# Optimization experiments

Hardware: AMD Instinct MI355X
Metric: run time of the kernel (lower is better)

Reference implementation:

```python
import jax, jax.numpy as jnp
import numpy as np

B, T, D, H, O = 1024, 256, 63, 128, 14


def _lstm_dir(x, W_ih, W_hh, b_ih, b_hh):
    """Single-direction LSTM over x [B,T,D] -> hidden outputs [B,T,H].
    PyTorch gate order: i, f, g, o."""
    # Precompute input projection for all timesteps (one big GEMM).
    xp = x @ W_ih.T + (b_ih + b_hh)  # [B,T,4H]

    def step(carry, xt):
        h, c = carry
        gates = xt + h @ W_hh.T  # [B,4H]
        i, f, g, o = jnp.split(gates, 4, axis=-1)
        i = jax.nn.sigmoid(i)
        f = jax.nn.sigmoid(f)
        g = jnp.tanh(g)
        o = jax.nn.sigmoid(o)
        c = f * c + i * g
        h = o * jnp.tanh(c)
        return (h, c), h

    h0 = jnp.zeros((x.shape[0], W_hh.shape[1]), x.dtype)
    (_, _), hs = jax.lax.scan(step, (h0, h0), jnp.swapaxes(xp, 0, 1))
    return jnp.swapaxes(hs, 0, 1)  # [B,T,H]


def setup_inputs() -> dict:
    key = jax.random.key(0)
    ks = jax.random.split(key, 11)
    s = 1.0 / np.sqrt(H)  # PyTorch LSTM init scale
    return {
        "x": jax.random.normal(ks[0], (B, T, D), jnp.float32),
        "W_ih_f": jax.random.uniform(ks[1], (4 * H, D), jnp.float32, -s, s),
        "W_hh_f": jax.random.uniform(ks[2], (4 * H, H), jnp.float32, -s, s),
        "b_ih_f": jax.random.uniform(ks[3], (4 * H,), jnp.float32, -s, s),
        "b_hh_f": jax.random.uniform(ks[4], (4 * H,), jnp.float32, -s, s),
        "W_ih_b": jax.random.uniform(ks[5], (4 * H, D), jnp.float32, -s, s),
        "W_hh_b": jax.random.uniform(ks[6], (4 * H, H), jnp.float32, -s, s),
        "b_ih_b": jax.random.uniform(ks[7], (4 * H,), jnp.float32, -s, s),
        "b_hh_b": jax.random.uniform(ks[8], (4 * H,), jnp.float32, -s, s),
        "W_fc": jax.random.uniform(ks[9], (O, 2 * H), jnp.float32, -s, s),
        "b_fc": jax.random.uniform(ks[10], (O,), jnp.float32, -s, s),
    }


def reference(x, W_ih_f, W_hh_f, b_ih_f, b_hh_f,
              W_ih_b, W_hh_b, b_ih_b, b_hh_b, W_fc, b_fc):
    h_f = _lstm_dir(x, W_ih_f, W_hh_f, b_ih_f, b_hh_f)            # fwd dir
    h_b = _lstm_dir(x[:, ::-1], W_ih_b, W_hh_b, b_ih_b, b_hh_b)[:, ::-1]  # bwd dir
    # out[:, -1, :] of the BiLSTM; dropout is identity at inference.
    last = jnp.concatenate([h_f[:, -1], h_b[:, -1]], axis=-1)  # [B, 2H]
    return last @ W_fc.T + b_fc  # [B, O]
```

## Files before the change

kernel.cpp:

```cpp
#include <hip/hip_runtime.h>

typedef __attribute__((ext_vector_type(8))) short bf16x8;
typedef __attribute__((ext_vector_type(4))) float f32x4;

#define BB 1024
#define TT 256
#define DD 63
#define HH 128
#define CHUNK 4
#define HSTR 160
#define XSTR 96

#define LDS_BARRIER() asm volatile("s_waitcnt lgkmcnt(0)\n\ts_barrier" ::: "memory")

__device__ __forceinline__ short f2bf(float f) {
  unsigned u = __builtin_bit_cast(unsigned, f);
  u = (u + 0x7FFFu + ((u >> 16) & 1u)) >> 16;
  return (short)u;
}
__device__ __forceinline__ float sigm(float x) {
  return __builtin_amdgcn_rcpf(1.f + __expf(-x));
}
__device__ __forceinline__ float tanh_fast(float x) {
  float e = __expf(2.f * x);
  return 1.f - 2.f * __builtin_amdgcn_rcpf(e + 1.f);
}

__global__ __launch_bounds__(512, 2)
void bilstm_fused_kernel(const float* __restrict__ X,
                         const float* __restrict__ Wih,
                         const float* __restrict__ Whh,
                         const float* __restrict__ bih,
                         const float* __restrict__ bhh,
                         const float* __restrict__ Wih_b,
                         const float* __restrict__ bih_b,
                         const float* __restrict__ bhh_b,
                         const float* __restrict__ Wfc,
                         const float* __restrict__ bfc,
                         float* __restrict__ out) {
  __shared__ __align__(16) short hbuf[2 * 4 * HSTR];
  __shared__ __align__(16) short xbuf[2 * 4 * XSTR];
  __shared__ __align__(16) float fst[4 * 256];
  __shared__ __align__(16) float xl[4 * 64];
  __shared__ __align__(16) float glb[4 * 512];

  const int tid  = threadIdx.x;
  const int wave = tid >> 6;
  const int lane = tid & 63;
  const int quad = lane >> 4;
  const int l15  = lane & 15;
  const int b0   = blockIdx.x * CHUNK;
  const int br   = l15 & 3;

  bf16x8 Ah[4][4];
  bf16x8 Axw[4][2];
  f32x4  bias[4];
#pragma unroll
  for (int g = 0; g < 4; ++g) {
    const int n = g * 128 + wave * 16 + l15;
    const float* wr = Whh + (size_t)n * HH;
#pragma unroll
    for (int ks = 0; ks < 4; ++ks) {
      const int k0 = ks * 32 + quad * 8;
      f32x4 w0 = *(const f32x4*)(wr + k0);
      f32x4 w1 = *(const f32x4*)(wr + k0 + 4);
      bf16x8 v;
#pragma unroll
      for (int jj = 0; jj < 4; ++jj) { v[jj] = f2bf(w0[jj]); v[4 + jj] = f2bf(w1[jj]); }
      Ah[g][ks] = v;
    }
    const float* xr = Wih + (size_t)n * DD;
#pragma unroll
    for (int ks = 0; ks < 2; ++ks) {
      const int k0 = ks * 32 + quad * 8;
      bf16x8 v;
#pragma unroll
      for (int jj = 0; jj < 8; ++jj) {
        const int k = k0 + jj;
        v[jj] = (k < DD) ? f2bf(xr[k]) : (short)0;
      }
      Axw[g][ks] = v;
    }
    const int cb = g * 128 + wave * 16 + quad * 4;
    f32x4 b1 = *(const f32x4*)&bih[cb];
    f32x4 b2 = *(const f32x4*)&bhh[cb];
    bias[g] = b1 + b2;
  }

  for (int i = tid; i < 2 * 4 * HSTR; i += 512) hbuf[i] = 0;
  if (tid >= CHUNK * DD && tid < 256) {
    const int rr = tid & 3;
    xbuf[rr * XSTR + DD] = 0;
    xbuf[4 * XSTR + rr * XSTR + DD] = 0;
  }

  const int xrow = tid / DD;
  const int xd   = tid - xrow * DD;
  const bool xthr = (tid < CHUNK * DD);
  const float* xptr = X + ((size_t)(b0 + xrow) * TT) * DD + xd;
  float xv_pend = 0.f;
  if (xthr) {
    xbuf[xrow * XSTR + xd] = f2bf(xptr[0]);
    xv_pend = xptr[DD];
    xptr += 2 * DD;
  }
  __syncthreads();

  float cc = 0.f, hv = 0.f;
  const int hcol = wave * 16 + quad * 4 + (l15 >> 2);
  const bool s0 = (l15 & 4) != 0;
  const bool s1 = (l15 & 8) != 0;

  for (int t = 0; t < TT; ++t) {
    const int xcur = (t & 1) * (4 * XSTR);
    const int hcur = (t & 1) * (4 * HSTR);

    float xv_new = 0.f;
    const bool pf2 = xthr && (t + 2 < TT);
    if (pf2) { xv_new = *xptr; xptr += DD; }

    bf16x8 Bh_[4], Bx_[2];
#pragma unroll
    for (int ks = 0; ks < 4; ++ks)
      Bh_[ks] = *(const bf16x8*)&hbuf[hcur + br * HSTR + ks * 32 + quad * 8];
#pragma unroll
    for (int ks = 0; ks < 2; ++ks)
      Bx_[ks] = *(const bf16x8*)&xbuf[xcur + br * XSTR + ks * 32 + quad * 8];

    float gact[4];
#pragma unroll
    for (int g = 0; g < 4; ++g) {
      f32x4 a = __builtin_amdgcn_mfma_f32_16x16x32_bf16(Ah[g][0], Bh_[0], bias[g], 0, 0, 0);
      a = __builtin_amdgcn_mfma_f32_16x16x32_bf16(Ah[g][1], Bh_[1], a, 0, 0, 0);
      a = __builtin_amdgcn_mfma_f32_16x16x32_bf16(Ah[g][2], Bh_[2], a, 0, 0, 0);
      a = __builtin_amdgcn_mfma_f32_16x16x32_bf16(Ah[g][3], Bh_[3], a, 0, 0, 0);
      a = __builtin_amdgcn_mfma_f32_16x16x32_bf16(Axw[g][0], Bx_[0], a, 0, 0, 0);
      a = __builtin_amdgcn_mfma_f32_16x16x32_bf16(Axw[g][1], Bx_[1], a, 0, 0, 0);
      const float a01 = s0 ? a[1] : a[0];
      const float a23 = s0 ? a[3] : a[2];
      const float v = s1 ? a23 : a01;
      gact[g] = (g == 2) ? tanh_fast(v) : sigm(v);
    }

    cc = gact[1] * cc + gact[0] * gact[2];
    hv = gact[3] * tanh_fast(cc);
    hbuf[(hcur ^ (4 * HSTR)) + br * HSTR + hcol] = f2bf(hv);

    if (xthr && (t + 1 < TT))
      xbuf[(xcur ^ (4 * XSTR)) + xrow * XSTR + xd] = f2bf(xv_pend);
    xv_pend = xv_new;
    LDS_BARRIER();
  }

  fst[br * 256 + hcol] = hv;
  if (xthr)
    xl[xrow * 64 + xd] = X[((size_t)(b0 + xrow) * TT + (TT - 1)) * DD + xd];
  __syncthreads();

  {
    const int n = tid;
    const float* wr = Wih_b + (size_t)n * DD;
    const float bb2 = bih_b[n] + bhh_b[n];
    float a0 = bb2, a1 = bb2, a2 = bb2, a3 = bb2;
    for (int k = 0; k < DD; ++k) {
      const float w = wr[k];
      a0 += w * xl[0 * 64 + k];
      a1 += w * xl[1 * 64 + k];
      a2 += w * xl[2 * 64 + k];
      a3 += w * xl[3 * 64 + k];
    }
    glb[0 * 512 + n] = a0;
    glb[1 * 512 + n] = a1;
    glb[2 * 512 + n] = a2;
    glb[3 * 512 + n] = a3;
  }
  __syncthreads();

  {
    const int b = tid >> 7, j = tid & 127;
    const float iv = sigm(glb[b * 512 + j]);
    const float gv = tanh_fast(glb[b * 512 + 256 + j]);
    const float ov = sigm(glb[b * 512 + 384 + j]);
    fst[b * 256 + 128 + j] = ov * tanh_fast(iv * gv);
  }
  __syncthreads();

  if (tid < CHUNK * 14) {
    const int rr = tid / 14, o = tid - rr * 14;
    const float* wr = Wfc + (size_t)o * (2 * HH);
    float acc = bfc[o];
#pragma unroll 16
    for (int k = 0; k < 2 * HH; ++k) acc += wr[k] * fst[rr * 256 + k];
    out[(size_t)(b0 + rr) * 14 + o] = acc;
  }
}

extern "C" void kernel_launch(void* const* d_in, const int* in_sizes, int n_in,
                              void* d_out, int out_size, void* d_ws, size_t ws_size,
                              hipStream_t stream) {
  const float* X     = (const float*)d_in[0];
  const float* Wih_f = (const float*)d_in[1];
  const float* Whh_f = (const float*)d_in[2];
  const float* bih_f = (const float*)d_in[3];
  const float* bhh_f = (const float*)d_in[4];
  const float* Wih_b = (const float*)d_in[5];
  const float* bih_b = (const float*)d_in[7];
  const float* bhh_b = (const float*)d_in[8];
  const float* Wfc   = (const float*)d_in[9];
  const float* bfc   = (const float*)d_in[10];
  float* out = (float*)d_out;

  bilstm_fused_kernel<<<BB / CHUNK, 512, 0, stream>>>(
      X, Wih_f, Whh_f, bih_f, bhh_f, Wih_b, bih_b, bhh_b, Wfc, bfc, out);
}
```

Baseline: 269.4 us.

## Batch input projection over 4-timestep chunks with full-width MFMA tiles

Moves the input projection off the per-step recurrence. For each chunk of 4 timesteps, x is staged into LDS as 16 columns (4 batch rows by 4 timesteps) and projected with full 16-wide MFMA tiles. The results, bias included, are stored in an fp32 LDS buffer. Each step then starts its 4-MFMA recurrent chain from the precomputed value, and the next chunk's projection is interleaved into the current chunk's steps. This shortens the dependent MFMA chain per gate and uses otherwise wasted MFMA columns, at the cost of more LDS, extra fp32 LDS reads per step and an extra barrier every 4 steps.

```diff
diff --git a/kernel.cpp b/kernel.cpp
--- a/kernel.cpp
+++ b/kernel.cpp
@@ -9,7 +9,9 @@
 #define HH 128
 #define CHUNK 4
 #define HSTR 160
-#define XSTR 96
+#define XSTR2 72
+#define NSTR4 520
+#define CT 4
 
 #define LDS_BARRIER() asm volatile("s_waitcnt lgkmcnt(0)\n\ts_barrier" ::: "memory")
 
@@ -39,7 +41,8 @@
                          const float* __restrict__ bfc,
                          float* __restrict__ out) {
   __shared__ __align__(16) short hbuf[2 * 4 * HSTR];
-  __shared__ __align__(16) short xbuf[2 * 4 * XSTR];
+  __shared__ __align__(16) float xpbuf[16 * NSTR4];
+  __shared__ __align__(16) short xstage[2 * 16 * XSTR2];
   __shared__ __align__(16) float fst[4 * 256];
   __shared__ __align__(16) float xl[4 * 64];
   __shared__ __align__(16) float glb[4 * 512];
@@ -51,6 +54,7 @@
   const int l15  = lane & 15;
   const int b0   = blockIdx.x * CHUNK;
   const int br   = l15 & 3;
+  const int p    = l15 >> 2;
 
   bf16x8 Ah[4][4];
   bf16x8 Axw[4][2];
@@ -88,73 +92,120 @@
   }
 
   for (int i = tid; i < 2 * 4 * HSTR; i += 512) hbuf[i] = 0;
-  if (tid >= CHUNK * DD && tid < 256) {
-    const int rr = tid & 3;
-    xbuf[rr * XSTR + DD] = 0;
-    xbuf[4 * XSTR + rr * XSTR + DD] = 0;
-  }
-
-  const int xrow = tid / DD;
-  const int xd   = tid - xrow * DD;
-  const bool xthr = (tid < CHUNK * DD);
-  const float* xptr = X + ((size_t)(b0 + xrow) * TT) * DD + xd;
-  float xv_pend = 0.f;
-  if (xthr) {
-    xbuf[xrow * XSTR + xd] = f2bf(xptr[0]);
-    xv_pend = xptr[DD];
-    xptr += 2 * DD;
+  if (tid < 32) {
+    const int bufc = tid >> 4, c = tid & 15;
+    xstage[bufc * 16 * XSTR2 + c * XSTR2 + DD] = 0;
+  }
+
+  const bool sthr = (tid < 252);
+  int so_[4];
+  const float* sx_[4];
+#pragma unroll
+  for (int j = 0; j < 4; ++j) {
+    const int e = tid + 252 * j;
+    const int c = e / DD, k = e - DD * c;
+    so_[j] = c * XSTR2 + k;
+    sx_[j] = X + ((size_t)(b0 + (c & 3)) * TT + (c >> 2)) * DD + k;
+  }
+
+  if (sthr) {
+#pragma unroll
+    for (int j = 0; j < 4; ++j) xstage[so_[j]] = f2bf(sx_[j][0]);
+  }
+  float xr1_[4];
+  if (sthr) {
+#pragma unroll
+    for (int j = 0; j < 4; ++j) xr1_[j] = sx_[j][CT * DD];
+  }
+  __syncthreads();
+#pragma unroll
+  for (int g = 0; g < 4; ++g) {
+    bf16x8 B0 = *(const bf16x8*)&xstage[l15 * XSTR2 + quad * 8];
+    bf16x8 B1 = *(const bf16x8*)&xstage[l15 * XSTR2 + 32 + quad * 8];
+    f32x4 px = __builtin_amdgcn_mfma_f32_16x16x32_bf16(Axw[g][0], B0, bias[g], 0, 0, 0);
+    px = __builtin_amdgcn_mfma_f32_16x16x32_bf16(Axw[g][1], B1, px, 0, 0, 0);
+    *(f32x4*)&xpbuf[l15 * NSTR4 + g * 128 + wave * 16 + quad * 4] = px;
+  }
+  if (sthr) {
+#pragma unroll
+    for (int j = 0; j < 4; ++j) xstage[16 * XSTR2 + so_[j]] = f2bf(xr1_[j]);
   }
   __syncthreads();
 
   float cc = 0.f, hv = 0.f;
-  const int hcol = wave * 16 + quad * 4 + (l15 >> 2);
+  const int hcol = wave * 16 + quad * 4 + p;
   const bool s0 = (l15 & 4) != 0;
   const bool s1 = (l15 & 8) != 0;
 
-  for (int t = 0; t < TT; ++t) {
-    const int xcur = (t & 1) * (4 * XSTR);
-    const int hcur = (t & 1) * (4 * HSTR);
-
-    float xv_new = 0.f;
-    const bool pf2 = xthr && (t + 2 < TT);
-    if (pf2) { xv_new = *xptr; xptr += DD; }
-
-    bf16x8 Bh_[4], Bx_[2];
-#pragma unroll
-    for (int ks = 0; ks < 4; ++ks)
-      Bh_[ks] = *(const bf16x8*)&hbuf[hcur + br * HSTR + ks * 32 + quad * 8];
-#pragma unroll
-    for (int ks = 0; ks < 2; ++ks)
-      Bx_[ks] = *(const bf16x8*)&xbuf[xcur + br * XSTR + ks * 32 + quad * 8];
-
-    float gact[4];
-#pragma unroll
-    for (int g = 0; g < 4; ++g) {
-      f32x4 a = __builtin_amdgcn_mfma_f32_16x16x32_bf16(Ah[g][0], Bh_[0], bias[g], 0, 0, 0);
-      a = __builtin_amdgcn_mfma_f32_16x16x32_bf16(Ah[g][1], Bh_[1], a, 0, 0, 0);
-      a = __builtin_amdgcn_mfma_f32_16x16x32_bf16(Ah[g][2], Bh_[2], a, 0, 0, 0);
-      a = __builtin_amdgcn_mfma_f32_16x16x32_bf16(Ah[g][3], Bh_[3], a, 0, 0, 0);
-      a = __builtin_amdgcn_mfma_f32_16x16x32_bf16(Axw[g][0], Bx_[0], a, 0, 0, 0);
-      a = __builtin_amdgcn_mfma_f32_16x16x32_bf16(Axw[g][1], Bx_[1], a, 0, 0, 0);
-      const float a01 = s0 ? a[1] : a[0];
-      const float a23 = s0 ? a[3] : a[2];
-      const float v = s1 ? a23 : a01;
-      gact[g] = (g == 2) ? tanh_fast(v) : sigm(v);
-    }
-
-    cc = gact[1] * cc + gact[0] * gact[2];
-    hv = gact[3] * tanh_fast(cc);
-    hbuf[(hcur ^ (4 * HSTR)) + br * HSTR + hcol] = f2bf(hv);
-
-    if (xthr && (t + 1 < TT))
-      xbuf[(xcur ^ (4 * XSTR)) + xrow * XSTR + xd] = f2bf(xv_pend);
-    xv_pend = xv_new;
-    LDS_BARRIER();
+  for (int cu = 0; cu < TT / CT; ++cu) {
+    const int t0 = cu * CT;
+    float xr_[4];
+    f32x4 pxp[4];
+#pragma unroll
+    for (int s = 0; s < CT; ++s) {
+      const int t = t0 + s;
+      const int hcur = (t & 1) * (4 * HSTR);
+
+      if (s == 0 && cu <= TT / CT - 3 && sthr) {
+#pragma unroll
+        for (int j = 0; j < 4; ++j) xr_[j] = sx_[j][(size_t)(t0 + 2 * CT) * DD];
+      }
+
+      bf16x8 Bh_[4];
+#pragma unroll
+      for (int ks = 0; ks < 4; ++ks)
+        Bh_[ks] = *(const bf16x8*)&hbuf[hcur + br * HSTR + ks * 32 + quad * 8];
+
+      if (cu < TT / CT - 1) {
+        const int xs = ((cu + 1) & 1) * (16 * XSTR2);
+        bf16x8 B0 = *(const bf16x8*)&xstage[xs + l15 * XSTR2 + quad * 8];
+        bf16x8 B1 = *(const bf16x8*)&xstage[xs + l15 * XSTR2 + 32 + quad * 8];
+        f32x4 px = __builtin_amdgcn_mfma_f32_16x16x32_bf16(Axw[s][0], B0, bias[s], 0, 0, 0);
+        pxp[s] = __builtin_amdgcn_mfma_f32_16x16x32_bf16(Axw[s][1], B1, px, 0, 0, 0);
+      }
+
+      float gact[4];
+#pragma unroll
+      for (int g = 0; g < 4; ++g) {
+        f32x4 ci = *(const f32x4*)&xpbuf[(s * 4 + br) * NSTR4 + g * 128 + wave * 16 + quad * 4];
+        f32x4 a = __builtin_amdgcn_mfma_f32_16x16x32_bf16(Ah[g][0], Bh_[0], ci, 0, 0, 0);
+        a = __builtin_amdgcn_mfma_f32_16x16x32_bf16(Ah[g][1], Bh_[1], a, 0, 0, 0);
+        a = __builtin_amdgcn_mfma_f32_16x16x32_bf16(Ah[g][2], Bh_[2], a, 0, 0, 0);
+        a = __builtin_amdgcn_mfma_f32_16x16x32_bf16(Ah[g][3], Bh_[3], a, 0, 0, 0);
+        const float a01 = s0 ? a[1] : a[0];
+        const float a23 = s0 ? a[3] : a[2];
+        const float v = s1 ? a23 : a01;
+        gact[g] = (g == 2) ? tanh_fast(v) : sigm(v);
+      }
+
+      cc = gact[1] * cc + gact[0] * gact[2];
+      hv = gact[3] * tanh_fast(cc);
+      hbuf[(hcur ^ (4 * HSTR)) + br * HSTR + hcol] = f2bf(hv);
+
+      if (s < CT - 1 || cu == TT / CT - 1) {
+        LDS_BARRIER();
+      } else {
+        LDS_BARRIER();
+#pragma unroll
+        for (int g = 0; g < 4; ++g)
+          *(f32x4*)&xpbuf[l15 * NSTR4 + g * 128 + wave * 16 + quad * 4] = pxp[g];
+        if (cu <= TT / CT - 3 && sthr) {
+          const int xd2 = (cu & 1) * (16 * XSTR2);
+#pragma unroll
+          for (int j = 0; j < 4; ++j) xstage[xd2 + so_[j]] = f2bf(xr_[j]);
+        }
+        LDS_BARRIER();
+      }
+    }
   }
 
   fst[br * 256 + hcol] = hv;
-  if (xthr)
-    xl[xrow * 64 + xd] = X[((size_t)(b0 + xrow) * TT + (TT - 1)) * DD + xd];
+  {
+    const int xrow = tid / DD;
+    const int xd   = tid - xrow * DD;
+    if (tid < CHUNK * DD)
+      xl[xrow * 64 + xd] = X[((size_t)(b0 + xrow) * TT + (TT - 1)) * DD + xd];
+  }
   __syncthreads();
 
   {
```

New measurement: 269.4 us. About the same (+0.0%).

## Precompute next-step input projection off the recurrent critical path

Applied to the files above, without the earlier changes.

Computes the input projection (W_ih·x plus bias) for step t+1 during step t and stores it in registers, so each step's dependent MFMA chain holds only the four hidden-state MFMAs per gate. The x staging pipeline goes one step deeper, with an extra prefetch, a shifted double-buffer index and a prologue that fills both buffers and computes the first projection. This shortens the serial latency between barriers, at the cost of 16 more accumulator registers and more involved buffer indexing.

```diff
diff --git a/kernel.cpp b/kernel.cpp
--- a/kernel.cpp
+++ b/kernel.cpp
@@ -101,10 +101,22 @@
   float xv_pend = 0.f;
   if (xthr) {
     xbuf[xrow * XSTR + xd] = f2bf(xptr[0]);
-    xv_pend = xptr[DD];
-    xptr += 2 * DD;
-  }
-  __syncthreads();
+    xbuf[4 * XSTR + xrow * XSTR + xd] = f2bf(xptr[DD]);
+    xv_pend = xptr[2 * DD];
+    xptr += 3 * DD;
+  }
+  __syncthreads();
+
+  f32x4 xC[4];
+  {
+    bf16x8 B0 = *(const bf16x8*)&xbuf[br * XSTR + quad * 8];
+    bf16x8 B1 = *(const bf16x8*)&xbuf[br * XSTR + 32 + quad * 8];
+#pragma unroll
+    for (int g = 0; g < 4; ++g) {
+      f32x4 px = __builtin_amdgcn_mfma_f32_16x16x32_bf16(Axw[g][0], B0, bias[g], 0, 0, 0);
+      xC[g] = __builtin_amdgcn_mfma_f32_16x16x32_bf16(Axw[g][1], B1, px, 0, 0, 0);
+    }
+  }
 
   float cc = 0.f, hv = 0.f;
   const int hcol = wave * 16 + quad * 4 + (l15 >> 2);
@@ -116,38 +128,41 @@
     const int hcur = (t & 1) * (4 * HSTR);
 
     float xv_new = 0.f;
-    const bool pf2 = xthr && (t + 2 < TT);
-    if (pf2) { xv_new = *xptr; xptr += DD; }
-
-    bf16x8 Bh_[4], Bx_[2];
+    const bool pf3 = xthr && (t + 3 < TT);
+    if (pf3) { xv_new = *xptr; xptr += DD; }
+
+    bf16x8 Bh_[4], Bx0, Bx1;
 #pragma unroll
     for (int ks = 0; ks < 4; ++ks)
       Bh_[ks] = *(const bf16x8*)&hbuf[hcur + br * HSTR + ks * 32 + quad * 8];
-#pragma unroll
-    for (int ks = 0; ks < 2; ++ks)
-      Bx_[ks] = *(const bf16x8*)&xbuf[xcur + br * XSTR + ks * 32 + quad * 8];
+    Bx0 = *(const bf16x8*)&xbuf[(xcur ^ (4 * XSTR)) + br * XSTR + quad * 8];
+    Bx1 = *(const bf16x8*)&xbuf[(xcur ^ (4 * XSTR)) + br * XSTR + 32 + quad * 8];
 
     float gact[4];
 #pragma unroll
     for (int g = 0; g < 4; ++g) {
-      f32x4 a = __builtin_amdgcn_mfma_f32_16x16x32_bf16(Ah[g][0], Bh_[0], bias[g], 0, 0, 0);
+      f32x4 a = __builtin_amdgcn_mfma_f32_16x16x32_bf16(Ah[g][0], Bh_[0], xC[g], 0, 0, 0);
       a = __builtin_amdgcn_mfma_f32_16x16x32_bf16(Ah[g][1], Bh_[1], a, 0, 0, 0);
       a = __builtin_amdgcn_mfma_f32_16x16x32_bf16(Ah[g][2], Bh_[2], a, 0, 0, 0);
       a = __builtin_amdgcn_mfma_f32_16x16x32_bf16(Ah[g][3], Bh_[3], a, 0, 0, 0);
-      a = __builtin_amdgcn_mfma_f32_16x16x32_bf16(Axw[g][0], Bx_[0], a, 0, 0, 0);
-      a = __builtin_amdgcn_mfma_f32_16x16x32_bf16(Axw[g][1], Bx_[1], a, 0, 0, 0);
       const float a01 = s0 ? a[1] : a[0];
       const float a23 = s0 ? a[3] : a[2];
       const float v = s1 ? a23 : a01;
       gact[g] = (g == 2) ? tanh_fast(v) : sigm(v);
     }
 
+#pragma unroll
+    for (int g = 0; g < 4; ++g) {
+      f32x4 px = __builtin_amdgcn_mfma_f32_16x16x32_bf16(Axw[g][0], Bx0, bias[g], 0, 0, 0);
+      xC[g] = __builtin_amdgcn_mfma_f32_16x16x32_bf16(Axw[g][1], Bx1, px, 0, 0, 0);
+    }
+
     cc = gact[1] * cc + gact[0] * gact[2];
     hv = gact[3] * tanh_fast(cc);
     hbuf[(hcur ^ (4 * HSTR)) + br * HSTR + hcol] = f2bf(hv);
 
-    if (xthr && (t + 1 < TT))
-      xbuf[(xcur ^ (4 * XSTR)) + xrow * XSTR + xd] = f2bf(xv_pend);
+    if (xthr && (t + 2 < TT))
+      xbuf[xcur + xrow * XSTR + xd] = f2bf(xv_pend);
     xv_pend = xv_new;
     LDS_BARRIER();
   }
```

Measured after the change: 266.0 us. No clear change (-1.2%).
